# Kernel tuning notes

Measured on AMD Instinct MI355X. Metric: run time of the kernel, lower is better.

## Reference

```python
import jax, jax.numpy as jnp
import numpy as np

HID = 51

def _lstm_cell(x, h, c, W_ih, W_hh, b_ih, b_hh):
    # PyTorch LSTMCell: gates ordered (i, f, g, o)
    gates = x @ W_ih.T + b_ih + h @ W_hh.T + b_hh  # [B, 4*HID]
    i, f, g, o = jnp.split(gates, 4, axis=-1)
    i = jax.nn.sigmoid(i)
    f = jax.nn.sigmoid(f)
    g = jnp.tanh(g)
    o = jax.nn.sigmoid(o)
    c_new = f * c + i * g
    h_new = o * jnp.tanh(c_new)
    return h_new, c_new


def setup_inputs() -> dict:
    key = jax.random.key(0)
    ks = jax.random.split(key, 12)
    B, T = 1024, 1024
    s = 1.0 / np.sqrt(HID)  # torch LSTMCell init scale
    d = {
        "x": jax.random.normal(ks[0], (B, T), dtype=jnp.float32),
        "W_ih0": jax.random.uniform(ks[1], (4 * HID, 1), jnp.float32, -s, s),
        "W_hh0": jax.random.uniform(ks[2], (4 * HID, HID), jnp.float32, -s, s),
        "b_ih0": jax.random.uniform(ks[3], (4 * HID,), jnp.float32, -s, s),
        "b_hh0": jax.random.uniform(ks[4], (4 * HID,), jnp.float32, -s, s),
        "W_ih1": jax.random.uniform(ks[5], (4 * HID, HID), jnp.float32, -s, s),
        "W_hh1": jax.random.uniform(ks[6], (4 * HID, HID), jnp.float32, -s, s),
        "b_ih1": jax.random.uniform(ks[7], (4 * HID,), jnp.float32, -s, s),
        "b_hh1": jax.random.uniform(ks[8], (4 * HID,), jnp.float32, -s, s),
        "W_lin": jax.random.uniform(ks[9], (1, HID), jnp.float32, -s, s),
        "b_lin": jax.random.uniform(ks[10], (1,), jnp.float32, -s, s),
    }
    return d


def reference(x, W_ih0, W_hh0, b_ih0, b_hh0, W_ih1, W_hh1, b_ih1, b_hh1, W_lin, b_lin):
    B, T = x.shape
    h0 = jnp.zeros((B, HID), x.dtype)
    c0 = jnp.zeros((B, HID), x.dtype)
    h1 = jnp.zeros((B, HID), x.dtype)
    c1 = jnp.zeros((B, HID), x.dtype)

    def step(carry, x_t):
        h0, c0, h1, c1 = carry
        h0, c0 = _lstm_cell(x_t, h0, c0, W_ih0, W_hh0, b_ih0, b_hh0)
        h1, c1 = _lstm_cell(h0, h1, c1, W_ih1, W_hh1, b_ih1, b_hh1)
        out_t = h1 @ W_lin.T + b_lin  # [B, 1]
        return (h0, c0, h1, c1), out_t

    xs = x.T[:, :, None]  # [T, B, 1] per-timestep inputs
    _, outs = jax.lax.scan(step, (h0, c0, h1, c1), xs)
    # outs: [T, B, 1] -> [B, T] (matches torch.stack(outputs,1).squeeze(2))
    return outs[:, :, 0].T
```

## Files before the change

kernel.cpp:

```cpp
#include <hip/hip_runtime.h>

#define HID 51
#define TLEN 1024
#define NBATCH 4
#define NW 7
#define NTH (NW * 64)

typedef _Float16 f16x8 __attribute__((ext_vector_type(8)));
typedef float    f32x4 __attribute__((ext_vector_type(4)));

#define LOG2E 1.4426950408889634f

__device__ __forceinline__ float frcp(float v){ return __builtin_amdgcn_rcpf(v); }
__device__ __forceinline__ float sigm2(float v){ return frcp(1.f + __builtin_amdgcn_exp2f(-v)); }
__device__ __forceinline__ float tanh_c(float c){
    return fmaf(2.f, frcp(1.f + __builtin_amdgcn_exp2f(-2.f*LOG2E*c)), -1.f);
}


__global__ __launch_bounds__(NTH)
void lstm2_mfma(const float* __restrict__ x,
                const float* __restrict__ W_ih0, const float* __restrict__ W_hh0,
                const float* __restrict__ b_ih0, const float* __restrict__ b_hh0,
                const float* __restrict__ W_ih1, const float* __restrict__ W_hh1,
                const float* __restrict__ b_ih1, const float* __restrict__ b_hh1,
                const float* __restrict__ W_lin, const float* __restrict__ b_lin,
                float* __restrict__ out)
{
    const int tid = threadIdx.x;
    const int w = tid >> 6;
    const int l = tid & 63;
    const int n = l & 15;
    const int p = l >> 4;

    __shared__ _Float16 H0[2][1024];
    __shared__ _Float16 H1[2][1024];
    __shared__ __align__(16) float PRE[2*HID*NBATCH*4];
    __shared__ float XS[NBATCH][1032];

    for (int i = tid; i < 1024; i += NTH){
        H0[0][i] = (_Float16)0.f; H0[1][i] = (_Float16)0.f;
        H1[0][i] = (_Float16)0.f; H1[1][i] = (_Float16)0.f;
    }
    const long long bb = (long long)blockIdx.x * NBATCH;
    for (int i = tid; i < NBATCH*TLEN; i += NTH){
        const int r = i >> 10, c = i & 1023;
        XS[r][c] = x[(bb + r)*TLEN + c];
    }

    f16x8 A0[2][2];
    f16x8 A1[2][4];
    int  jet[2]; bool stAt[2];
    #pragma unroll
    for (int t=0; t<2; ++t){
        const int tile = w + 7*t;
        const int ar = 16*tile + n;
        const int aj = ar >> 2, arr = ar & 3;
        const bool rowv = (aj < HID);
        const int orow = arr*HID + aj;
        const float gsc = (arr == 2) ? 2.f*LOG2E : LOG2E;
        #pragma unroll
        for (int kb=0; kb<2; ++kb){
            f16x8 hi;
            #pragma unroll
            for (int jj=0; jj<8; ++jj){
                const int k = kb*32 + 8*p + jj;
                const float wv = (rowv && k < HID) ? gsc * W_hh0[orow*HID + k] : 0.f;
                hi[jj] = (_Float16)wv;
            }
            A0[t][kb] = hi;
        }
        #pragma unroll
        for (int kb=0; kb<4; ++kb){
            f16x8 hi;
            #pragma unroll
            for (int jj=0; jj<8; ++jj){
                const int k = kb*32 + 8*p + jj;
                float wv = 0.f;
                if (rowv){
                    if (k < 64) { if (k < HID) wv = gsc * W_ih1[orow*HID + k]; }
                    else        { const int kk = k - 64; if (kk < HID) wv = gsc * W_hh1[orow*HID + kk]; }
                } else if (ar == 204 && k >= 64){
                    const int kk = k - 64; if (kk < HID) wv = W_lin[kk];
                }
                hi[jj] = (_Float16)wv;
            }
            A1[t][kb] = hi;
        }
        jet[t]  = 4*tile + p;
        stAt[t] = (n < NBATCH) && (jet[t] < HID);
    }
    const bool outm = (w == 5) && (p == 3) && (n < NBATCH);
    const float blin = b_lin[0];

    const int q = tid;
    const bool eact = (q < 2*HID*NBATCH);
    const int lay = (q >= HID*NBATCH) ? 1 : 0;
    const int qq = q - lay*HID*NBATCH;
    const int jq = qq >> 2, nq = qq & 3;
    f32x4 biasq = {0.f,0.f,0.f,0.f}, wxq = {0.f,0.f,0.f,0.f};
    if (eact){
        const float* bi = lay ? b_ih1 : b_ih0;
        const float* bh = lay ? b_hh1 : b_hh0;
        #pragma unroll
        for (int r4=0; r4<4; ++r4){
            const float gs4 = (r4 == 2) ? 2.f*LOG2E : LOG2E;
            const int oe = r4*HID + jq;
            biasq[r4] = gs4 * (bi[oe] + bh[oe]);
            if (!lay) wxq[r4] = gs4 * W_ih0[oe];
        }
    }
    const int widxq = ((jq>>5)<<9) + (nq + ((jq>>3)&3)*16)*8 + (jq&7);
    float cst = 0.f;

    __syncthreads();

    for (int s = 0; s <= TLEN + 1; ++s){
        const int pw = s & 1, pr = pw ^ 1;

        f16x8 rb[2], r1[2];
        #pragma unroll
        for (int kb=0; kb<2; ++kb){
            rb[kb] = *reinterpret_cast<const f16x8*>(&H0[pr][kb*512 + l*8]);
            r1[kb] = *reinterpret_cast<const f16x8*>(&H1[pw][kb*512 + l*8]);
        }
        if (s < TLEN){
            __builtin_amdgcn_s_setprio(1);
            f32x4 a0 = {0.f,0.f,0.f,0.f}, a1 = {0.f,0.f,0.f,0.f};
            a0 = __builtin_amdgcn_mfma_f32_16x16x32_f16(A0[0][0], rb[0], a0, 0,0,0);
            a1 = __builtin_amdgcn_mfma_f32_16x16x32_f16(A0[1][0], rb[0], a1, 0,0,0);
            a0 = __builtin_amdgcn_mfma_f32_16x16x32_f16(A0[0][1], rb[1], a0, 0,0,0);
            a1 = __builtin_amdgcn_mfma_f32_16x16x32_f16(A0[1][1], rb[1], a1, 0,0,0);
            __builtin_amdgcn_s_setprio(0);
            if (stAt[0]) *reinterpret_cast<f32x4*>(&PRE[(jet[0]*NBATCH + n)*4]) = a0;
            if (stAt[1]) *reinterpret_cast<f32x4*>(&PRE[(jet[1]*NBATCH + n)*4]) = a1;
        }
        if (s >= 1){
            __builtin_amdgcn_s_setprio(1);
            f32x4 b0 = {0.f,0.f,0.f,0.f}, b1 = {0.f,0.f,0.f,0.f};
            f32x4 c0 = {0.f,0.f,0.f,0.f}, c1 = {0.f,0.f,0.f,0.f};
            b0 = __builtin_amdgcn_mfma_f32_16x16x32_f16(A1[0][0], rb[0], b0, 0,0,0);
            c0 = __builtin_amdgcn_mfma_f32_16x16x32_f16(A1[1][0], rb[0], c0, 0,0,0);
            b1 = __builtin_amdgcn_mfma_f32_16x16x32_f16(A1[0][2], r1[0], b1, 0,0,0);
            c1 = __builtin_amdgcn_mfma_f32_16x16x32_f16(A1[1][2], r1[0], c1, 0,0,0);
            b0 = __builtin_amdgcn_mfma_f32_16x16x32_f16(A1[0][1], rb[1], b0, 0,0,0);
            c0 = __builtin_amdgcn_mfma_f32_16x16x32_f16(A1[1][1], rb[1], c0, 0,0,0);
            b1 = __builtin_amdgcn_mfma_f32_16x16x32_f16(A1[0][3], r1[1], b1, 0,0,0);
            c1 = __builtin_amdgcn_mfma_f32_16x16x32_f16(A1[1][3], r1[1], c1, 0,0,0);
            __builtin_amdgcn_s_setprio(0);
            const f32x4 preT0 = b0 + b1;
            const f32x4 preT1 = c0 + c1;
            if (s <= TLEN){
                if (stAt[0]) *reinterpret_cast<f32x4*>(&PRE[(HID*NBATCH + jet[0]*NBATCH + n)*4]) = preT0;
                if (stAt[1]) *reinterpret_cast<f32x4*>(&PRE[(HID*NBATCH + jet[1]*NBATCH + n)*4]) = preT1;
            }
            if (outm && s >= 2)
                out[(bb + n)*TLEN + (s-2)] = preT1[0] + blin;
        }
        __syncthreads();

        if (eact && (lay ? (s >= 1 && s <= TLEN) : (s < TLEN))){
            f32x4 pre = *reinterpret_cast<const f32x4*>(&PRE[q*4]);
            pre += biasq;
            if (!lay){
                const float xq = XS[nq][s];
                #pragma unroll
                for (int r4=0; r4<4; ++r4) pre[r4] = fmaf(xq, wxq[r4], pre[r4]);
            }
            const float gi = sigm2(pre[0]);
            const float gf = sigm2(pre[1]);
            const float gg = fmaf(2.f, sigm2(pre[2]), -1.f);
            const float go = sigm2(pre[3]);
            cst = fmaf(gf, cst, gi*gg);
            const float hv = go * tanh_c(cst);
            if (lay) H1[pr][widxq] = (_Float16)hv;
            else     H0[pw][widxq] = (_Float16)hv;
        }
        __syncthreads();
    }
}

extern "C" void kernel_launch(void* const* d_in, const int* in_sizes, int n_in,
                              void* d_out, int out_size, void* d_ws, size_t ws_size,
                              hipStream_t stream) {
    const float* x     = (const float*)d_in[0];
    const float* W_ih0 = (const float*)d_in[1];
    const float* W_hh0 = (const float*)d_in[2];
    const float* b_ih0 = (const float*)d_in[3];
    const float* b_hh0 = (const float*)d_in[4];
    const float* W_ih1 = (const float*)d_in[5];
    const float* W_hh1 = (const float*)d_in[6];
    const float* b_ih1 = (const float*)d_in[7];
    const float* b_hh1 = (const float*)d_in[8];
    const float* W_lin = (const float*)d_in[9];
    const float* b_lin = (const float*)d_in[10];
    float* out = (float*)d_out;

    const int B = in_sizes[0] / TLEN;
    lstm2_mfma<<<dim3(B / NBATCH), dim3(NTH), 0, stream>>>(
        x, W_ih0, W_hh0, b_ih0, b_hh0, W_ih1, W_hh1, b_ih1, b_hh1, W_lin, b_lin, out);
}
```

Measured before the change: 733.3 us.

## Replace block barriers with LDS counter spin-waits and fold bias into MFMA accumulators

Swaps the two __syncthreads per timestep for per-wave atomic increments on shared counters plus volatile spin-waits. It also initializes the MFMA accumulators with the bias and input-projection terms, so the elementwise phase no longer adds them. The aim is lower barrier overhead and fewer ops on the serial recurrence path. The spin-waits cost LDS traffic and rely on memory-ordering assumptions. Counters are reset by thread 0 before the first __syncthreads, which is sound.

Result: slower. 937.0 us (+27.8%).

```diff
diff --git a/kernel.cpp b/kernel.cpp
--- a/kernel.cpp
+++ b/kernel.cpp
@@ -37,6 +37,7 @@
     __shared__ _Float16 H1[2][1024];
     __shared__ __align__(16) float PRE[2*HID*NBATCH*4];
     __shared__ float XS[NBATCH][1032];
+    __shared__ unsigned CNT_A, CNT_B;
 
     for (int i = tid; i < 1024; i += NTH){
         H0[0][i] = (_Float16)0.f; H0[1][i] = (_Float16)0.f;
@@ -47,9 +48,11 @@
         const int r = i >> 10, c = i & 1023;
         XS[r][c] = x[(bb + r)*TLEN + c];
     }
+    if (tid == 0){ CNT_A = 0u; CNT_B = 0u; }
 
     f16x8 A0[2][2];
     f16x8 A1[2][4];
+    f32x4 b0c[2], wx0c[2], b1c[2];
     int  jet[2]; bool stAt[2];
     #pragma unroll
     for (int t=0; t<2; ++t){
@@ -89,6 +92,16 @@
         }
         jet[t]  = 4*tile + p;
         stAt[t] = (n < NBATCH) && (jet[t] < HID);
+        const int je = jet[t];
+        const bool jev = (je < HID) && (tile < 13);
+        #pragma unroll
+        for (int r4=0; r4<4; ++r4){
+            const float gs4 = (r4 == 2) ? 2.f*LOG2E : LOG2E;
+            const int oe = r4*HID + je;
+            b0c[t][r4]  = jev ? gs4 * (b_ih0[oe] + b_hh0[oe]) : 0.f;
+            wx0c[t][r4] = jev ? gs4 * W_ih0[oe] : 0.f;
+            b1c[t][r4]  = jev ? gs4 * (b_ih1[oe] + b_hh1[oe]) : 0.f;
+        }
     }
     const bool outm = (w == 5) && (p == 3) && (n < NBATCH);
     const float blin = b_lin[0];
@@ -98,18 +111,6 @@
     const int lay = (q >= HID*NBATCH) ? 1 : 0;
     const int qq = q - lay*HID*NBATCH;
     const int jq = qq >> 2, nq = qq & 3;
-    f32x4 biasq = {0.f,0.f,0.f,0.f}, wxq = {0.f,0.f,0.f,0.f};
-    if (eact){
-        const float* bi = lay ? b_ih1 : b_ih0;
-        const float* bh = lay ? b_hh1 : b_hh0;
-        #pragma unroll
-        for (int r4=0; r4<4; ++r4){
-            const float gs4 = (r4 == 2) ? 2.f*LOG2E : LOG2E;
-            const int oe = r4*HID + jq;
-            biasq[r4] = gs4 * (bi[oe] + bh[oe]);
-            if (!lay) wxq[r4] = gs4 * W_ih0[oe];
-        }
-    }
     const int widxq = ((jq>>5)<<9) + (nq + ((jq>>3)&3)*16)*8 + (jq&7);
     float cst = 0.f;
 
@@ -117,6 +118,7 @@
 
     for (int s = 0; s <= TLEN + 1; ++s){
         const int pw = s & 1, pr = pw ^ 1;
+        const unsigned tgt = 7u * (unsigned)(s + 1);
 
         f16x8 rb[2], r1[2];
         #pragma unroll
@@ -124,9 +126,15 @@
             rb[kb] = *reinterpret_cast<const f16x8*>(&H0[pr][kb*512 + l*8]);
             r1[kb] = *reinterpret_cast<const f16x8*>(&H1[pw][kb*512 + l*8]);
         }
+        const float xv = XS[n & 3][s & 1023];
         if (s < TLEN){
+            f32x4 a0 = b0c[0], a1 = b0c[1];
+            #pragma unroll
+            for (int r4=0; r4<4; ++r4){
+                a0[r4] = fmaf(xv, wx0c[0][r4], a0[r4]);
+                a1[r4] = fmaf(xv, wx0c[1][r4], a1[r4]);
+            }
             __builtin_amdgcn_s_setprio(1);
-            f32x4 a0 = {0.f,0.f,0.f,0.f}, a1 = {0.f,0.f,0.f,0.f};
             a0 = __builtin_amdgcn_mfma_f32_16x16x32_f16(A0[0][0], rb[0], a0, 0,0,0);
             a1 = __builtin_amdgcn_mfma_f32_16x16x32_f16(A0[1][0], rb[0], a1, 0,0,0);
             a0 = __builtin_amdgcn_mfma_f32_16x16x32_f16(A0[0][1], rb[1], a0, 0,0,0);
@@ -137,8 +145,8 @@
         }
         if (s >= 1){
             __builtin_amdgcn_s_setprio(1);
-            f32x4 b0 = {0.f,0.f,0.f,0.f}, b1 = {0.f,0.f,0.f,0.f};
-            f32x4 c0 = {0.f,0.f,0.f,0.f}, c1 = {0.f,0.f,0.f,0.f};
+            f32x4 b0 = b1c[0], b1 = {0.f,0.f,0.f,0.f};
+            f32x4 c0 = b1c[1], c1 = {0.f,0.f,0.f,0.f};
             b0 = __builtin_amdgcn_mfma_f32_16x16x32_f16(A1[0][0], rb[0], b0, 0,0,0);
             c0 = __builtin_amdgcn_mfma_f32_16x16x32_f16(A1[1][0], rb[0], c0, 0,0,0);
             b1 = __builtin_amdgcn_mfma_f32_16x16x32_f16(A1[0][2], r1[0], b1, 0,0,0);
@@ -157,16 +165,14 @@
             if (outm && s >= 2)
                 out[(bb + n)*TLEN + (s-2)] = preT1[0] + blin;
         }
-        __syncthreads();
+        __threadfence_block();
+        if (l == 0) atomicAdd(&CNT_A, 1u);
+        while (*(volatile unsigned*)&CNT_A < tgt) {}
+        __builtin_amdgcn_sched_barrier(0);
+        asm volatile("" ::: "memory");
 
         if (eact && (lay ? (s >= 1 && s <= TLEN) : (s < TLEN))){
-            f32x4 pre = *reinterpret_cast<const f32x4*>(&PRE[q*4]);
-            pre += biasq;
-            if (!lay){
-                const float xq = XS[nq][s];
-                #pragma unroll
-                for (int r4=0; r4<4; ++r4) pre[r4] = fmaf(xq, wxq[r4], pre[r4]);
-            }
+            const f32x4 pre = *reinterpret_cast<const f32x4*>(&PRE[q*4]);
             const float gi = sigm2(pre[0]);
             const float gf = sigm2(pre[1]);
             const float gg = fmaf(2.f, sigm2(pre[2]), -1.f);
@@ -176,7 +182,11 @@
             if (lay) H1[pr][widxq] = (_Float16)hv;
             else     H0[pw][widxq] = (_Float16)hv;
         }
-        __syncthreads();
+        __threadfence_block();
+        if (l == 0) atomicAdd(&CNT_B, 1u);
+        while (*(volatile unsigned*)&CNT_B < tgt) {}
+        __builtin_amdgcn_sched_barrier(0);
+        asm volatile("" ::: "memory");
     }
 }
 
```
